# Kernel optimization log

Hardware: AMD Instinct MI355X
Metric: run time of the kernel (lower is better)

Reference implementation:

```python
import jax, jax.numpy as jnp
import numpy as np

HEADS = 8


def setup_inputs() -> dict:
    key = jax.random.key(0)
    k1, k2, k3 = jax.random.split(key, 3)
    b, n, d = 4, 2048, 256
    x = jax.random.normal(k1, (b, n, d), dtype=jnp.float32)
    # torch Linear weight is [out, in]; we store transposed [in, out] for x @ W
    w_qkv = jax.random.normal(k2, (d, 3 * d), dtype=jnp.float32) * (d ** -0.5)
    b_qkv = jnp.zeros((3 * d,), dtype=jnp.float32)
    w_out = jax.random.normal(k3, (d, d), dtype=jnp.float32) * (d ** -0.5)
    b_out = jnp.zeros((d,), dtype=jnp.float32)
    return {"x": x, "w_qkv": w_qkv, "b_qkv": b_qkv, "w_out": w_out, "b_out": b_out}


def reference(x, w_qkv, b_qkv, w_out, b_out):
    b, n, d = x.shape
    h = HEADS
    dh = d // h
    scale = d ** -0.5  # NOTE: original scales by full dim**-0.5, not head_dim
    qkv = x @ w_qkv + b_qkv                      # [b, n, 3d]
    q, k, v = jnp.split(qkv, 3, axis=-1)         # each [b, n, d]
    to_heads = lambda t: t.reshape(b, n, h, dh).transpose(0, 2, 1, 3)  # [b,h,n,dh]
    q, k, v = to_heads(q), to_heads(k), to_heads(v)
    dots = jnp.einsum('bhid,bhjd->bhij', q, k) * scale   # [b,h,n,n]
    attn = jax.nn.softmax(dots, axis=-1)
    out = jnp.einsum('bhij,bhjd->bhid', attn, v)         # [b,h,n,dh]
    out = out.transpose(0, 2, 1, 3).reshape(b, n, d)     # [b,n,d]
    return out @ w_out + b_out  # dropout is identity in eval mode
```

## Files before the change

### kernel.cpp

```cpp
#include <hip/hip_runtime.h>
#include <hip/hip_bf16.h>
#include <math.h>

#define BATCH  4
#define SEQ    2048
#define DMODEL 256
#define NH     8
#define DH     32
#define MTOT   (BATCH*SEQ)
#define QSCALE 0.09016844005556021f

typedef short  bf16x8 __attribute__((ext_vector_type(8)));
typedef float  f32x4  __attribute__((ext_vector_type(4)));

static __device__ __forceinline__ ushort f2bf(float f) {
    __hip_bfloat16 h = __float2bfloat16(f);
    return __builtin_bit_cast(ushort, h);
}
static __device__ __forceinline__ uint rne2(float a, float b) {
    uint ua = __builtin_bit_cast(uint, a);
    uint ub = __builtin_bit_cast(uint, b);
    ua += 0x7FFFu + ((ua >> 16) & 1u);
    ub += 0x7FFFu + ((ub >> 16) & 1u);
    return __builtin_amdgcn_perm(ub, ua, 0x07060302);
}
static __device__ __forceinline__ uint pk2(float a, float b) {
#if __has_builtin(__builtin_amdgcn_cvt_pk_bf16_f32)
    auto r = __builtin_amdgcn_cvt_pk_bf16_f32(a, b);
    return __builtin_bit_cast(uint, r);
#else
    return rne2(a, b);
#endif
}

static __device__ __forceinline__ uint e2pk(float a, float b) {
    return pk2(__builtin_amdgcn_exp2f(a), __builtin_amdgcn_exp2f(b));
}

static __device__ __forceinline__ bf16x8 redist(uint t0lo, uint t0hi,
                                                uint t1lo, uint t1hi,
                                                int lane) {
#if __has_builtin(__builtin_amdgcn_permlane32_swap) && __has_builtin(__builtin_amdgcn_permlane16_swap)
    auto rl = __builtin_amdgcn_permlane32_swap(t0lo, t1lo, false, false);
    auto rh = __builtin_amdgcn_permlane32_swap(t0hi, t1hi, false, false);
    auto sl = __builtin_amdgcn_permlane16_swap(rl[0], rl[1], false, false);
    auto sh = __builtin_amdgcn_permlane16_swap(rh[0], rh[1], false, false);
    uint4 pw = {sl[0], sh[0], sl[1], sh[1]};
#else
    uint a0 = __shfl_xor((int)t0lo, 32), b0 = __shfl_xor((int)t1lo, 32);
    uint a1 = __shfl_xor((int)t0hi, 32), b1 = __shfl_xor((int)t1hi, 32);
    uint Xl = (lane & 32) ? b0 : t0lo,  Yl = (lane & 32) ? t1lo : a0;
    uint Xh = (lane & 32) ? b1 : t0hi,  Yh = (lane & 32) ? t1hi : a1;
    uint sXl = __shfl_xor((int)Xl, 16), sYl = __shfl_xor((int)Yl, 16);
    uint sXh = __shfl_xor((int)Xh, 16), sYh = __shfl_xor((int)Yh, 16);
    uint4 pw = {(lane & 16) ? sYl : Xl, (lane & 16) ? sYh : Xh,
                (lane & 16) ? Yl : sXl, (lane & 16) ? Yh : sXh};
#endif
    return __builtin_bit_cast(bf16x8, pw);
}

#define LSQ 72

__global__ __launch_bounds__(256) void wcvt_all(
    const float* __restrict__ wq, const float* __restrict__ wo,
    const float* __restrict__ x,
    ushort* __restrict__ wqT, ushort* __restrict__ woT,
    ushort* __restrict__ xbf)
{
    const int t  = threadIdx.x;
    const int bx = blockIdx.x;
    if (bx >= 32) {
        const size_t base = ((size_t)(bx - 32) * 8 + blockIdx.y) * 4096 + t * 16;
        float4 f0 = *(const float4*)(x + base);
        float4 f1 = *(const float4*)(x + base + 4);
        float4 f2 = *(const float4*)(x + base + 8);
        float4 f3 = *(const float4*)(x + base + 12);
        uint4 w0, w1;
        w0.x = pk2(f0.x, f0.y); w0.y = pk2(f0.z, f0.w);
        w0.z = pk2(f1.x, f1.y); w0.w = pk2(f1.z, f1.w);
        w1.x = pk2(f2.x, f2.y); w1.y = pk2(f2.z, f2.w);
        w1.z = pk2(f3.x, f3.y); w1.w = pk2(f3.z, f3.w);
        *(uint4*)&xbf[base]     = w0;
        *(uint4*)&xbf[base + 8] = w1;
        return;
    }
    __shared__ float T[32][33];
    const float* w; ushort* wT; int N, n0;
    if (bx < 24) { w = wq; wT = wqT; N = 768; n0 = bx * 32; }
    else         { w = wo; wT = woT; N = 256; n0 = (bx - 24) * 32; }
    const int k0 = blockIdx.y * 32;
    {
        int tr = t >> 3, tc = (t & 7) * 4;
        *(float4*)&T[tr][tc] = *(const float4*)(w + (size_t)(k0 + tr) * N + n0 + tc);
    }
    __syncthreads();
    int nl = t >> 3, kq = (t & 7) * 4;
    ushort4 pk;
    pk.x = f2bf(T[kq + 0][nl]); pk.y = f2bf(T[kq + 1][nl]);
    pk.z = f2bf(T[kq + 2][nl]); pk.w = f2bf(T[kq + 3][nl]);
    *(ushort4*)&wT[(size_t)(n0 + nl) * 256 + k0 + kq] = pk;
}

__global__ __launch_bounds__(256, 3) void qkv_gemm(
    const ushort* __restrict__ xb_, const ushort* __restrict__ wT,
    const float* __restrict__ bias,
    ushort* __restrict__ qo, ushort* __restrict__ ko, ushort* __restrict__ vo)
{
    __shared__ ushort As[64 * LSQ];
    __shared__ ushort Bs[128 * LSQ];
    const int tid  = threadIdx.x;
    const int wid  = tid >> 6;
    const int lane = tid & 63;
    const int lq   = lane & 15;
    const int quad = lane >> 4;
    const int wm   = wid & 1;
    const int wn   = wid >> 1;
    const int m0   = blockIdx.y * 64;
    const int n0   = blockIdx.x * 128;
    const bool isV = (blockIdx.x >= 4);

    const int ar0 = tid >> 3,         ac0 = (tid & 7) * 8;
    const int ar1 = (tid + 256) >> 3;
    const int br0 = tid >> 3,         bc0 = (tid & 7) * 8;
    const int br1 = (tid + 256) >> 3;
    const int br2 = (tid + 512) >> 3;
    const int br3 = (tid + 768) >> 3;

    const ushort* xb = xb_ + (size_t)m0 * 256;
    const ushort* wb = wT  + (size_t)n0 * 256;

    f32x4 acc[8];
#pragma unroll
    for (int i = 0; i < 8; ++i) acc[i] = {0.f, 0.f, 0.f, 0.f};

    uint4 ra0 = *(const uint4*)(xb + (size_t)ar0 * 256 + ac0);
    uint4 ra1 = *(const uint4*)(xb + (size_t)ar1 * 256 + ac0);
    uint4 rb0 = *(const uint4*)(wb + (size_t)br0 * 256 + bc0);
    uint4 rb1 = *(const uint4*)(wb + (size_t)br1 * 256 + bc0);
    uint4 rb2 = *(const uint4*)(wb + (size_t)br2 * 256 + bc0);
    uint4 rb3 = *(const uint4*)(wb + (size_t)br3 * 256 + bc0);

    for (int k0 = 0; k0 < 256; k0 += 64) {
        __syncthreads();
        *(uint4*)&As[ar0 * LSQ + ac0] = ra0;
        *(uint4*)&As[ar1 * LSQ + ac0] = ra1;
        *(uint4*)&Bs[br0 * LSQ + bc0] = rb0;
        *(uint4*)&Bs[br1 * LSQ + bc0] = rb1;
        *(uint4*)&Bs[br2 * LSQ + bc0] = rb2;
        *(uint4*)&Bs[br3 * LSQ + bc0] = rb3;
        __syncthreads();

        const int kn = (k0 + 64) & 255;
        ra0 = *(const uint4*)(xb + (size_t)ar0 * 256 + kn + ac0);
        ra1 = *(const uint4*)(xb + (size_t)ar1 * 256 + kn + ac0);
        rb0 = *(const uint4*)(wb + (size_t)br0 * 256 + kn + bc0);
        rb1 = *(const uint4*)(wb + (size_t)br1 * 256 + kn + bc0);
        rb2 = *(const uint4*)(wb + (size_t)br2 * 256 + kn + bc0);
        rb3 = *(const uint4*)(wb + (size_t)br3 * 256 + kn + bc0);

#pragma unroll
        for (int kh = 0; kh < 2; ++kh) {
            bf16x8 af[2], bfg[4];
#pragma unroll
            for (int mi = 0; mi < 2; ++mi)
                af[mi]  = *(const bf16x8*)&As[(wm * 32 + mi * 16 + lq) * LSQ + kh * 32 + quad * 8];
#pragma unroll
            for (int ni = 0; ni < 4; ++ni)
                bfg[ni] = *(const bf16x8*)&Bs[(wn * 64 + ni * 16 + lq) * LSQ + kh * 32 + quad * 8];
            if (isV) {
#pragma unroll
                for (int mi = 0; mi < 2; ++mi)
#pragma unroll
                    for (int ni = 0; ni < 4; ++ni)
                        acc[mi * 4 + ni] = __builtin_amdgcn_mfma_f32_16x16x32_bf16(
                            af[mi], bfg[ni], acc[mi * 4 + ni], 0, 0, 0);
            } else {
#pragma unroll
                for (int ni = 0; ni < 4; ++ni)
#pragma unroll
                    for (int mi = 0; mi < 2; ++mi)
                        acc[ni * 2 + mi] = __builtin_amdgcn_mfma_f32_16x16x32_bf16(
                            bfg[ni], af[mi], acc[ni * 2 + mi], 0, 0, 0);
            }
        }
    }

    if (!isV) {
#pragma unroll
        for (int ni = 0; ni < 4; ++ni) {
            int nb = n0 + wn * 64 + ni * 16 + quad * 4;
            float4 bs = *(const float4*)(bias + nb);
            int h   = (nb >> 5) & 7;
            int dh0 = nb & 31;
            bool  isQ = (nb < 256);
            float sc  = isQ ? QSCALE : 1.0f;
            ushort* dst = isQ ? qo : ko;
#pragma unroll
            for (int mi = 0; mi < 2; ++mi) {
                int m   = m0 + wm * 32 + mi * 16 + lq;
                int b   = m >> 11, seq = m & 2047;
                f32x4 c = acc[ni * 2 + mi];
                ushort4 pk;
                pk.x = f2bf((c[0] + bs.x) * sc); pk.y = f2bf((c[1] + bs.y) * sc);
                pk.z = f2bf((c[2] + bs.z) * sc); pk.w = f2bf((c[3] + bs.w) * sc);
                *(ushort4*)&dst[(((size_t)b * NH + h) * SEQ + seq) * DH + dh0] = pk;
            }
        }
    } else {
#pragma unroll
        for (int ni = 0; ni < 4; ++ni) {
            int n  = n0 + wn * 64 + ni * 16 + lq;
            int h  = (n >> 5) & 7;
            int dh = n & 31;
            float bsc = bias[n];
#pragma unroll
            for (int mi = 0; mi < 2; ++mi) {
                int mb  = m0 + wm * 32 + mi * 16 + quad * 4;
                int b   = mb >> 11, seq = mb & 2047;
                f32x4 c = acc[mi * 4 + ni];
                ushort4 pk;
                pk.x = f2bf(c[0] + bsc); pk.y = f2bf(c[1] + bsc);
                pk.z = f2bf(c[2] + bsc); pk.w = f2bf(c[3] + bsc);
                *(ushort4*)&vo[(((size_t)b * NH + h) * DH + dh) * SEQ + seq] = pk;
            }
        }
    }
}

__global__ __launch_bounds__(256, 5) void attn_mfma(
    const ushort* __restrict__ qb, const ushort* __restrict__ kb,
    const ushort* __restrict__ vtb, ushort* __restrict__ a_bf)
{
    __shared__ float Red[3][64][20];

    const int tid  = threadIdx.x;
    const int wid  = tid >> 6;
    const int lane = tid & 63;
    const int lq   = lane & 15;
    const int quad = lane >> 4;

    const int lin = blockIdx.x + (blockIdx.y << 6) + (blockIdx.z << 9);
    const int swz = ((lin & 7) << 8) | (lin >> 3);
    const int qc  = swz & 63;
    const int h   = (swz >> 6) & 7;
    const int b   = swz >> 9;
    const int bh  = b * NH + h;
    const int q0  = qc * 32;

    const ushort* qbase = qb + ((size_t)bh * SEQ + q0) * DH;
    const bf16x8 qf0 = *(const bf16x8*)(qbase + (size_t)lq * DH + quad * 8);
    const bf16x8 qf1 = *(const bf16x8*)(qbase + (size_t)(16 + lq) * DH + quad * 8);

    const ushort* kp = kb  + ((size_t)bh * SEQ + wid * 512 + lq) * DH + quad * 8;
    const ushort* vp = vtb + ((size_t)bh * DH + lq) * SEQ + wid * 512 + quad * 8;

    f32x4 o0 = {0.f,0.f,0.f,0.f}, o1 = {0.f,0.f,0.f,0.f};
    f32x4 o2 = {0.f,0.f,0.f,0.f}, o3 = {0.f,0.f,0.f,0.f};
    f32x4 la0 = {0.f,0.f,0.f,0.f}, la1 = {0.f,0.f,0.f,0.f};
    const bf16x8 ones = {0x3F80, 0x3F80, 0x3F80, 0x3F80,
                         0x3F80, 0x3F80, 0x3F80, 0x3F80};

#pragma unroll 4
    for (int kt = 0; kt < 512; kt += 32) {
        bf16x8 kf0 = *(const bf16x8*)(kp + (size_t)kt * DH);
        bf16x8 kf1 = *(const bf16x8*)(kp + (size_t)(kt + 16) * DH);
        bf16x8 v0  = *(const bf16x8*)(vp + kt);
        bf16x8 v1  = *(const bf16x8*)(vp + 16 * SEQ + kt);

        f32x4 z = {0.f, 0.f, 0.f, 0.f};
        f32x4 sa0 = __builtin_amdgcn_mfma_f32_16x16x32_bf16(kf0, qf0, z, 0, 0, 0);
        f32x4 sa1 = __builtin_amdgcn_mfma_f32_16x16x32_bf16(kf1, qf0, z, 0, 0, 0);
        f32x4 sb0 = __builtin_amdgcn_mfma_f32_16x16x32_bf16(kf0, qf1, z, 0, 0, 0);
        f32x4 sb1 = __builtin_amdgcn_mfma_f32_16x16x32_bf16(kf1, qf1, z, 0, 0, 0);

        bf16x8 p0 = redist(e2pk(sa0[0], sa0[1]), e2pk(sa0[2], sa0[3]),
                           e2pk(sa1[0], sa1[1]), e2pk(sa1[2], sa1[3]), lane);
        bf16x8 p1 = redist(e2pk(sb0[0], sb0[1]), e2pk(sb0[2], sb0[3]),
                           e2pk(sb1[0], sb1[1]), e2pk(sb1[2], sb1[3]), lane);

        o0  = __builtin_amdgcn_mfma_f32_16x16x32_bf16(v0,   p0, o0,  0, 0, 0);
        o1  = __builtin_amdgcn_mfma_f32_16x16x32_bf16(v1,   p0, o1,  0, 0, 0);
        o2  = __builtin_amdgcn_mfma_f32_16x16x32_bf16(v0,   p1, o2,  0, 0, 0);
        o3  = __builtin_amdgcn_mfma_f32_16x16x32_bf16(v1,   p1, o3,  0, 0, 0);
        la0 = __builtin_amdgcn_mfma_f32_16x16x32_bf16(ones, p0, la0, 0, 0, 0);
        la1 = __builtin_amdgcn_mfma_f32_16x16x32_bf16(ones, p1, la1, 0, 0, 0);
    }

    if (wid) {
        float* r = &Red[wid - 1][lane][0];
        *(f32x4*)&r[0]  = o0;  *(f32x4*)&r[4]  = o1;
        *(f32x4*)&r[8]  = o2;  *(f32x4*)&r[12] = o3;
        r[16] = la0[0]; r[17] = la1[0];
    }
    __syncthreads();
    if (wid == 0) {
        float l0 = la0[0], l1 = la1[0];
#pragma unroll
        for (int j = 0; j < 3; ++j) {
            const float* r = &Red[j][lane][0];
            f32x4 a0 = *(const f32x4*)&r[0],  a1 = *(const f32x4*)&r[4];
            f32x4 a2 = *(const f32x4*)&r[8],  a3 = *(const f32x4*)&r[12];
            o0 += a0; o1 += a1; o2 += a2; o3 += a3;
            l0 += r[16]; l1 += r[17];
        }
        float inv0 = 1.0f / l0;
        float inv1 = 1.0f / l1;

        ushort* dst0 = a_bf + ((size_t)b * SEQ + q0 + lq) * DMODEL + h * DH;
        ushort* dst1 = dst0 + 16 * DMODEL;
        uint2 w0, w1;
        w0.x = pk2(o0[0] * inv0, o0[1] * inv0);
        w0.y = pk2(o0[2] * inv0, o0[3] * inv0);
        w1.x = pk2(o1[0] * inv0, o1[1] * inv0);
        w1.y = pk2(o1[2] * inv0, o1[3] * inv0);
        *(uint2*)&dst0[quad * 4]      = w0;
        *(uint2*)&dst0[16 + quad * 4] = w1;
        w0.x = pk2(o2[0] * inv1, o2[1] * inv1);
        w0.y = pk2(o2[2] * inv1, o2[3] * inv1);
        w1.x = pk2(o3[0] * inv1, o3[1] * inv1);
        w1.y = pk2(o3[2] * inv1, o3[3] * inv1);
        *(uint2*)&dst1[quad * 4]      = w0;
        *(uint2*)&dst1[16 + quad * 4] = w1;
    }
}

__global__ __launch_bounds__(256) void out_gemm(
    const ushort* __restrict__ a, const ushort* __restrict__ wT,
    const float* __restrict__ bias, float* __restrict__ out)
{
    __shared__ ushort As[64 * LSQ];
    __shared__ ushort Bs[64 * LSQ];
    const int tid  = threadIdx.x;
    const int wid  = tid >> 6;
    const int lane = tid & 63;
    const int lq   = lane & 15;
    const int quad = lane >> 4;
    const int wm   = wid & 1;
    const int wn   = wid >> 1;
    const int m0   = blockIdx.y * 64;
    const int n0   = blockIdx.x * 64;

    const int f0 = tid, f1 = tid + 256;
    const int r0 = f0 >> 3, c0 = (f0 & 7) * 8;
    const int r1 = f1 >> 3, c1 = (f1 & 7) * 8;

    const ushort* ab = a  + (size_t)m0 * 256;
    const ushort* wb = wT + (size_t)n0 * 256;

    f32x4 acc[4];
#pragma unroll
    for (int i = 0; i < 4; ++i) acc[i] = {0.f, 0.f, 0.f, 0.f};

    uint4 ra0 = *(const uint4*)(ab + (size_t)r0 * 256 + c0);
    uint4 ra1 = *(const uint4*)(ab + (size_t)r1 * 256 + c1);
    uint4 rb0 = *(const uint4*)(wb + (size_t)r0 * 256 + c0);
    uint4 rb1 = *(const uint4*)(wb + (size_t)r1 * 256 + c1);

    for (int k0 = 0; k0 < 256; k0 += 64) {
        __syncthreads();
        *(uint4*)&As[r0 * LSQ + c0] = ra0;
        *(uint4*)&As[r1 * LSQ + c1] = ra1;
        *(uint4*)&Bs[r0 * LSQ + c0] = rb0;
        *(uint4*)&Bs[r1 * LSQ + c1] = rb1;
        __syncthreads();

        const int kn = (k0 + 64) & 255;
        ra0 = *(const uint4*)(ab + (size_t)r0 * 256 + kn + c0);
        ra1 = *(const uint4*)(ab + (size_t)r1 * 256 + kn + c1);
        rb0 = *(const uint4*)(wb + (size_t)r0 * 256 + kn + c0);
        rb1 = *(const uint4*)(wb + (size_t)r1 * 256 + kn + c1);

#pragma unroll
        for (int kh = 0; kh < 2; ++kh) {
            bf16x8 af[2], bfg[2];
#pragma unroll
            for (int mi = 0; mi < 2; ++mi)
                af[mi]  = *(const bf16x8*)&As[(wm * 32 + mi * 16 + lq) * LSQ + kh * 32 + quad * 8];
#pragma unroll
            for (int ni = 0; ni < 2; ++ni)
                bfg[ni] = *(const bf16x8*)&Bs[(wn * 32 + ni * 16 + lq) * LSQ + kh * 32 + quad * 8];
#pragma unroll
            for (int ni = 0; ni < 2; ++ni)
#pragma unroll
                for (int mi = 0; mi < 2; ++mi)
                    acc[ni * 2 + mi] = __builtin_amdgcn_mfma_f32_16x16x32_bf16(
                        bfg[ni], af[mi], acc[ni * 2 + mi], 0, 0, 0);
        }
    }

#pragma unroll
    for (int ni = 0; ni < 2; ++ni) {
        int nb = n0 + wn * 32 + ni * 16 + quad * 4;
        float4 bs = *(const float4*)(bias + nb);
#pragma unroll
        for (int mi = 0; mi < 2; ++mi) {
            int m = m0 + wm * 32 + mi * 16 + lq;
            f32x4 c = acc[ni * 2 + mi];
            float4 o;
            o.x = c[0] + bs.x; o.y = c[1] + bs.y;
            o.z = c[2] + bs.z; o.w = c[3] + bs.w;
            *(float4*)&out[(size_t)m * DMODEL + nb] = o;
        }
    }
}

extern "C" void kernel_launch(void* const* d_in, const int* in_sizes, int n_in,
                              void* d_out, int out_size, void* d_ws, size_t ws_size,
                              hipStream_t stream) {
    const float* x     = (const float*)d_in[0];
    const float* w_qkv = (const float*)d_in[1];
    const float* b_qkv = (const float*)d_in[2];
    const float* w_out = (const float*)d_in[3];
    const float* b_out = (const float*)d_in[4];
    float* out = (float*)d_out;

    const size_t TSZ = (size_t)MTOT * DMODEL;
    ushort* q_ws = (ushort*)d_ws;
    ushort* k_ws = q_ws + TSZ;
    ushort* v_ws = k_ws + TSZ;
    ushort* a_bf = v_ws + TSZ;
    ushort* xbf  = a_bf + TSZ;
    ushort* wqT  = xbf + TSZ;
    ushort* woT  = wqT + 768 * 256;

    wcvt_all<<<dim3(96, 8), 256, 0, stream>>>(w_qkv, w_out, x, wqT, woT, xbf);
    qkv_gemm<<<dim3(6, 128), 256, 0, stream>>>(xbf, wqT, b_qkv, q_ws, k_ws, v_ws);
    attn_mfma<<<dim3(64, NH, BATCH), 256, 0, stream>>>(
        q_ws, k_ws, v_ws, a_bf);
    out_gemm<<<dim3(4, 128), 256, 0, stream>>>(a_bf, woT, b_out, out);
}
```

Before: 130.8 us.

## Stage K/V tiles in shared memory and share them across two query chunks

The attention kernel now uses 512-thread blocks that each handle two 32-query chunks with four key quarters per chunk. K and V^T tiles are loaded cooperatively into padded LDS with a register prefetch of the next tile, so every global K/V load is reused by two query chunks instead of each wave reading global memory directly. The cost is two barriers per tile, extra LDS traffic and fewer blocks. The cross-wave reduction buffer now reuses the same LDS.

```diff
diff --git a/kernel.cpp b/kernel.cpp
--- a/kernel.cpp
+++ b/kernel.cpp
@@ -227,32 +227,56 @@
     }
 }
 
-__global__ __launch_bounds__(256, 5) void attn_mfma(
+__global__ __launch_bounds__(512, 4) void attn_mfma(
     const ushort* __restrict__ qb, const ushort* __restrict__ kb,
     const ushort* __restrict__ vtb, ushort* __restrict__ a_bf)
 {
-    __shared__ float Red[3][64][20];
+    __shared__ ushort SM[19456];
 
     const int tid  = threadIdx.x;
     const int wid  = tid >> 6;
     const int lane = tid & 63;
     const int lq   = lane & 15;
     const int quad = lane >> 4;
-
-    const int lin = blockIdx.x + (blockIdx.y << 6) + (blockIdx.z << 9);
-    const int swz = ((lin & 7) << 8) | (lin >> 3);
-    const int qc  = swz & 63;
-    const int h   = (swz >> 6) & 7;
-    const int b   = swz >> 9;
+    const int qc   = wid & 1;
+    const int quarter = wid >> 1;
+
+    const int lin = blockIdx.x + (blockIdx.y << 5) + (blockIdx.z << 8);
+    const int swz = ((lin & 7) << 7) | (lin >> 3);
+    const int qpair = swz & 31;
+    const int h   = (swz >> 5) & 7;
+    const int b   = swz >> 8;
     const int bh  = b * NH + h;
-    const int q0  = qc * 32;
+    const int q0  = qpair * 64 + qc * 32;
 
     const ushort* qbase = qb + ((size_t)bh * SEQ + q0) * DH;
     const bf16x8 qf0 = *(const bf16x8*)(qbase + (size_t)lq * DH + quad * 8);
     const bf16x8 qf1 = *(const bf16x8*)(qbase + (size_t)(16 + lq) * DH + quad * 8);
 
-    const ushort* kp = kb  + ((size_t)bh * SEQ + wid * 512 + lq) * DH + quad * 8;
-    const ushort* vp = vtb + ((size_t)bh * DH + lq) * SEQ + wid * 512 + quad * 8;
+    const ushort* kbase  = kb  + (size_t)bh * SEQ * DH;
+    const ushort* vtbase = vtb + (size_t)bh * DH * SEQ;
+
+    const int kv0 = tid, kv1 = tid + 512;
+    const int kq0 = kv0 >> 8, kr0 = (kv0 & 255) >> 2, kc0 = (kv0 & 3) * 8;
+    const int kq1 = kv1 >> 8, kr1 = (kv1 & 255) >> 2, kc1 = (kv1 & 3) * 8;
+    const int gk0 = (kq0 * 512 + kr0) * DH + kc0;
+    const int gk1 = (kq1 * 512 + kr1) * DH + kc1;
+    const int lk0 = kq0 * 2560 + kr0 * 40 + kc0;
+    const int lk1 = kq1 * 2560 + kr1 * 40 + kc1;
+    const int vq0 = kv0 >> 8, vr0 = (kv0 & 255) >> 3, vc0 = (kv0 & 7) * 8;
+    const int vq1 = kv1 >> 8, vr1 = (kv1 & 255) >> 3, vc1 = (kv1 & 7) * 8;
+    const int gv0 = vr0 * SEQ + vq0 * 512 + vc0;
+    const int gv1 = vr1 * SEQ + vq1 * 512 + vc1;
+    const int lv0 = 10240 + vq0 * 2304 + vr0 * 72 + vc0;
+    const int lv1 = 10240 + vq1 * 2304 + vr1 * 72 + vc1;
+
+    uint4 fka = *(const uint4*)(kbase + gk0);
+    uint4 fkb = *(const uint4*)(kbase + gk1);
+    uint4 fva = *(const uint4*)(vtbase + gv0);
+    uint4 fvb = *(const uint4*)(vtbase + gv1);
+
+    const ushort* Kq = SM + quarter * 2560;
+    const ushort* Vq = SM + 10240 + quarter * 2304;
 
     f32x4 o0 = {0.f,0.f,0.f,0.f}, o1 = {0.f,0.f,0.f,0.f};
     f32x4 o2 = {0.f,0.f,0.f,0.f}, o3 = {0.f,0.f,0.f,0.f};
@@ -260,44 +284,63 @@
     const bf16x8 ones = {0x3F80, 0x3F80, 0x3F80, 0x3F80,
                          0x3F80, 0x3F80, 0x3F80, 0x3F80};
 
-#pragma unroll 4
-    for (int kt = 0; kt < 512; kt += 32) {
-        bf16x8 kf0 = *(const bf16x8*)(kp + (size_t)kt * DH);
-        bf16x8 kf1 = *(const bf16x8*)(kp + (size_t)(kt + 16) * DH);
-        bf16x8 v0  = *(const bf16x8*)(vp + kt);
-        bf16x8 v1  = *(const bf16x8*)(vp + 16 * SEQ + kt);
-
-        f32x4 z = {0.f, 0.f, 0.f, 0.f};
-        f32x4 sa0 = __builtin_amdgcn_mfma_f32_16x16x32_bf16(kf0, qf0, z, 0, 0, 0);
-        f32x4 sa1 = __builtin_amdgcn_mfma_f32_16x16x32_bf16(kf1, qf0, z, 0, 0, 0);
-        f32x4 sb0 = __builtin_amdgcn_mfma_f32_16x16x32_bf16(kf0, qf1, z, 0, 0, 0);
-        f32x4 sb1 = __builtin_amdgcn_mfma_f32_16x16x32_bf16(kf1, qf1, z, 0, 0, 0);
-
-        bf16x8 p0 = redist(e2pk(sa0[0], sa0[1]), e2pk(sa0[2], sa0[3]),
-                           e2pk(sa1[0], sa1[1]), e2pk(sa1[2], sa1[3]), lane);
-        bf16x8 p1 = redist(e2pk(sb0[0], sb0[1]), e2pk(sb0[2], sb0[3]),
-                           e2pk(sb1[0], sb1[1]), e2pk(sb1[2], sb1[3]), lane);
-
-        o0  = __builtin_amdgcn_mfma_f32_16x16x32_bf16(v0,   p0, o0,  0, 0, 0);
-        o1  = __builtin_amdgcn_mfma_f32_16x16x32_bf16(v1,   p0, o1,  0, 0, 0);
-        o2  = __builtin_amdgcn_mfma_f32_16x16x32_bf16(v0,   p1, o2,  0, 0, 0);
-        o3  = __builtin_amdgcn_mfma_f32_16x16x32_bf16(v1,   p1, o3,  0, 0, 0);
-        la0 = __builtin_amdgcn_mfma_f32_16x16x32_bf16(ones, p0, la0, 0, 0, 0);
-        la1 = __builtin_amdgcn_mfma_f32_16x16x32_bf16(ones, p1, la1, 0, 0, 0);
-    }
-
-    if (wid) {
-        float* r = &Red[wid - 1][lane][0];
+    for (int t = 0; t < 8; ++t) {
+        __syncthreads();
+        *(uint4*)&SM[lk0] = fka;
+        *(uint4*)&SM[lk1] = fkb;
+        *(uint4*)&SM[lv0] = fva;
+        *(uint4*)&SM[lv1] = fvb;
+        __syncthreads();
+
+        {
+            const int tn = (t + 1) & 7;
+            fka = *(const uint4*)(kbase + (size_t)tn * 64 * DH + gk0);
+            fkb = *(const uint4*)(kbase + (size_t)tn * 64 * DH + gk1);
+            fva = *(const uint4*)(vtbase + tn * 64 + gv0);
+            fvb = *(const uint4*)(vtbase + tn * 64 + gv1);
+        }
+
+#pragma unroll
+        for (int s = 0; s < 2; ++s) {
+            bf16x8 kf0 = *(const bf16x8*)&Kq[(s * 32 + lq) * 40 + quad * 8];
+            bf16x8 kf1 = *(const bf16x8*)&Kq[(s * 32 + 16 + lq) * 40 + quad * 8];
+            f32x4 z = {0.f, 0.f, 0.f, 0.f};
+            f32x4 sa0 = __builtin_amdgcn_mfma_f32_16x16x32_bf16(kf0, qf0, z, 0, 0, 0);
+            f32x4 sa1 = __builtin_amdgcn_mfma_f32_16x16x32_bf16(kf1, qf0, z, 0, 0, 0);
+            f32x4 sb0 = __builtin_amdgcn_mfma_f32_16x16x32_bf16(kf0, qf1, z, 0, 0, 0);
+            f32x4 sb1 = __builtin_amdgcn_mfma_f32_16x16x32_bf16(kf1, qf1, z, 0, 0, 0);
+
+            bf16x8 v0 = *(const bf16x8*)&Vq[lq        * 72 + s * 32 + quad * 8];
+            bf16x8 v1 = *(const bf16x8*)&Vq[(16 + lq) * 72 + s * 32 + quad * 8];
+
+            bf16x8 p0 = redist(e2pk(sa0[0], sa0[1]), e2pk(sa0[2], sa0[3]),
+                               e2pk(sa1[0], sa1[1]), e2pk(sa1[2], sa1[3]), lane);
+            bf16x8 p1 = redist(e2pk(sb0[0], sb0[1]), e2pk(sb0[2], sb0[3]),
+                               e2pk(sb1[0], sb1[1]), e2pk(sb1[2], sb1[3]), lane);
+
+            o0  = __builtin_amdgcn_mfma_f32_16x16x32_bf16(v0,   p0, o0,  0, 0, 0);
+            o1  = __builtin_amdgcn_mfma_f32_16x16x32_bf16(v1,   p0, o1,  0, 0, 0);
+            o2  = __builtin_amdgcn_mfma_f32_16x16x32_bf16(v0,   p1, o2,  0, 0, 0);
+            o3  = __builtin_amdgcn_mfma_f32_16x16x32_bf16(v1,   p1, o3,  0, 0, 0);
+            la0 = __builtin_amdgcn_mfma_f32_16x16x32_bf16(ones, p0, la0, 0, 0, 0);
+            la1 = __builtin_amdgcn_mfma_f32_16x16x32_bf16(ones, p1, la1, 0, 0, 0);
+        }
+    }
+
+    __syncthreads();
+    float* Red = (float*)SM;
+    if (quarter) {
+        float* r = &Red[(((qc * 3) + quarter - 1) * 64 + lane) * 20];
         *(f32x4*)&r[0]  = o0;  *(f32x4*)&r[4]  = o1;
         *(f32x4*)&r[8]  = o2;  *(f32x4*)&r[12] = o3;
         r[16] = la0[0]; r[17] = la1[0];
     }
     __syncthreads();
-    if (wid == 0) {
+    if (quarter == 0) {
         float l0 = la0[0], l1 = la1[0];
 #pragma unroll
         for (int j = 0; j < 3; ++j) {
-            const float* r = &Red[j][lane][0];
+            const float* r = &Red[(((qc * 3) + j) * 64 + lane) * 20];
             f32x4 a0 = *(const f32x4*)&r[0],  a1 = *(const f32x4*)&r[4];
             f32x4 a2 = *(const f32x4*)&r[8],  a3 = *(const f32x4*)&r[12];
             o0 += a0; o1 += a1; o2 += a2; o3 += a3;
@@ -425,7 +468,7 @@
 
     wcvt_all<<<dim3(96, 8), 256, 0, stream>>>(w_qkv, w_out, x, wqT, woT, xbf);
     qkv_gemm<<<dim3(6, 128), 256, 0, stream>>>(xbf, wqT, b_qkv, q_ws, k_ws, v_ws);
-    attn_mfma<<<dim3(64, NH, BATCH), 256, 0, stream>>>(
+    attn_mfma<<<dim3(32, NH, BATCH), 512, 0, stream>>>(
         q_ws, k_ws, v_ws, a_bf);
     out_gemm<<<dim3(4, 128), 256, 0, stream>>>(a_bf, woT, b_out, out);
 }
```

After: 122.1 us. 6.6% less time.
